# Performance work log

Hardware: AMD Instinct MI355X
Metric: run time of the kernel (lower is better)

## Reference

```python
import jax, jax.numpy as jnp
import numpy as np

B, N, D = 8, 4096, 3


def setup_inputs() -> dict:
    key = jax.random.key(0)
    k1, k2, k3 = jax.random.split(key, 3)
    pred1 = jax.random.normal(k1, (B, N, D), dtype=jnp.float32)
    pred2 = jax.random.normal(k2, (B, N, D), dtype=jnp.float32)
    # weighted adjacency in [0,1); column sums (degrees) strictly > 0
    A = jax.random.uniform(k3, (B, N, N), dtype=jnp.float32)
    return {"pred1": pred1, "pred2": pred2, "A": A}


def _centroid(x, A):
    # torch code computes neighbours[b,i,d] = sum_j A[b,i,j] * x[b,j,d]
    # and divides by num_neighbours[b,i] = sum over dim=1 of A (column sums).
    deg = jnp.sum(A, axis=1)                     # [B, N] column sums
    neigh = jnp.einsum('bij,bjd->bid', A, x)     # [B, N, D] row-aggregation
    return neigh / deg[..., None]


def reference(pred1, pred2, A):
    lap1 = pred1 - _centroid(pred1, A)
    lap2 = pred2 - _centroid(pred2, A)
    d = lap2 - lap1
    return jnp.sum(d * d)
```

## Files before the change

### kernel.cpp

```cpp
#include <hip/hip_runtime.h>

#define BB 8
#define NN 4096
#define TPB 256
#define NCB 32
#define SC 128
#define NRB 4
#define RR 1024
#define TSTEPS (RR / 16)
#define NDSLAB (NRB * 4)


__global__ __launch_bounds__(256) void k_init(const float* __restrict__ p1,
                                              const float* __restrict__ p2,
                                              float* __restrict__ q,
                                              float* __restrict__ neighp,
                                              float* __restrict__ degp,
                                              float* __restrict__ out,
                                              int atomic_mode) {
    int i = blockIdx.x * 256 + threadIdx.x;
    if (i < BB * NN * 3) q[i] = p2[i] - p1[i];
    if (atomic_mode) {
        if (i < BB * NN * 3) neighp[i] = 0.0f;
        if (i < BB * NN) degp[i] = 0.0f;
    }
    if (i == 0) out[0] = 0.0f;
}

__global__ __launch_bounds__(TPB, 4) void k_main(const float* __restrict__ A,
                                                 const float* __restrict__ q,
                                                 float* __restrict__ neighp,
                                                 float* __restrict__ degp,
                                                 int atomic_mode) {
    const int lane = threadIdx.x & 63;
    const int w    = threadIdx.x >> 6;
    const int rs   = lane >> 4;
    const int cq   = lane & 15;

    int bid = blockIdx.x;
    const int cb = bid & (NCB - 1); bid >>= 5;
    const int rb = bid & (NRB - 1); bid >>= 2;
    const int b  = bid;

    const int col  = cb * SC + cq * 8;
    const int row0 = rb * RR + w * 4 + rs;

    const float* qp = q + (size_t)b * NN * 3 + (size_t)col * 3;
    const float4 v0 = *(const float4*)(qp + 0);
    const float4 v1 = *(const float4*)(qp + 4);
    const float4 v2 = *(const float4*)(qp + 8);
    const float4 v3 = *(const float4*)(qp + 12);
    const float4 v4 = *(const float4*)(qp + 16);
    const float4 v5 = *(const float4*)(qp + 20);

    const float* Ap = A + (size_t)b * NN * NN + (size_t)row0 * NN + col;

    float4 dgA = make_float4(0.f, 0.f, 0.f, 0.f);
    float4 dgB = make_float4(0.f, 0.f, 0.f, 0.f);

    float* npbase = atomic_mode ? (neighp + (size_t)b * NN * 3)
                                : (neighp + (size_t)(cb * BB + b) * NN * 3);

#pragma unroll 2
    for (int t = 0; t < TSTEPS; ++t) {
        const float4 a1 = *(const float4*)(Ap);
        const float4 a2 = *(const float4*)(Ap + 4);
        Ap += (size_t)16 * NN;

        dgA.x += a1.x; dgA.y += a1.y; dgA.z += a1.z; dgA.w += a1.w;
        dgB.x += a2.x; dgB.y += a2.y; dgB.z += a2.z; dgB.w += a2.w;

        float n0 = a1.x * v0.x + a1.y * v0.w + a1.z * v1.z + a1.w * v2.y +
                   a2.x * v3.x + a2.y * v3.w + a2.z * v4.z + a2.w * v5.y;
        float n1 = a1.x * v0.y + a1.y * v1.x + a1.z * v1.w + a1.w * v2.z +
                   a2.x * v3.y + a2.y * v4.x + a2.z * v4.w + a2.w * v5.z;
        float n2 = a1.x * v0.z + a1.y * v1.y + a1.z * v2.x + a1.w * v2.w +
                   a2.x * v3.z + a2.y * v4.y + a2.z * v5.x + a2.w * v5.w;

#pragma unroll
        for (int s = 1; s < 16; s <<= 1) {
            n0 += __shfl_xor(n0, s, 64);
            n1 += __shfl_xor(n1, s, 64);
            n2 += __shfl_xor(n2, s, 64);
        }
        if (cq == 0) {
            const int row = row0 + t * 16;
            float* p = npbase + (size_t)row * 3;
            if (atomic_mode) {
                atomicAdd(&p[0], n0); atomicAdd(&p[1], n1); atomicAdd(&p[2], n2);
            } else {
                p[0] = n0; p[1] = n1; p[2] = n2;
            }
        }
    }

#pragma unroll
    for (int s = 16; s < 64; s <<= 1) {
        dgA.x += __shfl_xor(dgA.x, s, 64); dgA.y += __shfl_xor(dgA.y, s, 64);
        dgA.z += __shfl_xor(dgA.z, s, 64); dgA.w += __shfl_xor(dgA.w, s, 64);
        dgB.x += __shfl_xor(dgB.x, s, 64); dgB.y += __shfl_xor(dgB.y, s, 64);
        dgB.z += __shfl_xor(dgB.z, s, 64); dgB.w += __shfl_xor(dgB.w, s, 64);
    }
    if (rs == 0) {
        if (atomic_mode) {
            float* dp = degp + (size_t)b * NN + col;
            atomicAdd(&dp[0], dgA.x); atomicAdd(&dp[1], dgA.y);
            atomicAdd(&dp[2], dgA.z); atomicAdd(&dp[3], dgA.w);
            atomicAdd(&dp[4], dgB.x); atomicAdd(&dp[5], dgB.y);
            atomicAdd(&dp[6], dgB.z); atomicAdd(&dp[7], dgB.w);
        } else {
            float* dp = degp + ((size_t)(rb * 4 + w) * BB + b) * NN + col;
            *(float4*)(dp + 0) = dgA;
            *(float4*)(dp + 4) = dgB;
        }
    }
}

__global__ __launch_bounds__(256) void k_final(const float* __restrict__ q,
                                               const float* __restrict__ neighp,
                                               const float* __restrict__ degp,
                                               int nslab, int ncb,
                                               float* __restrict__ out) {
    __shared__ float dredN[4][64][3];
    __shared__ float dredD[4][64];
    const int lane = threadIdx.x & 63;
    const int qi   = threadIdx.x >> 6;
    const int R    = blockIdx.x * 64 + lane;
    const int b    = R / NN;
    const int i    = R - b * NN;

    float n0 = 0.f, n1 = 0.f, n2 = 0.f;
    for (int c = qi; c < ncb; c += 4) {
        const float* p = neighp + ((size_t)(c * BB + b) * NN + i) * 3;
        n0 += p[0]; n1 += p[1]; n2 += p[2];
    }
    dredN[qi][lane][0] = n0; dredN[qi][lane][1] = n1; dredN[qi][lane][2] = n2;

    float d0 = 0.f;
    for (int s = qi; s < nslab; s += 4)
        d0 += degp[((size_t)s * BB + b) * NN + i];
    dredD[qi][lane] = d0;
    __syncthreads();

    if (qi == 0) {
        const float deg = dredD[0][lane] + dredD[1][lane] + dredD[2][lane] + dredD[3][lane];
        const float inv = 1.0f / deg;
        const float nd0 = dredN[0][lane][0] + dredN[1][lane][0] + dredN[2][lane][0] + dredN[3][lane][0];
        const float nd1 = dredN[0][lane][1] + dredN[1][lane][1] + dredN[2][lane][1] + dredN[3][lane][1];
        const float nd2 = dredN[0][lane][2] + dredN[1][lane][2] + dredN[2][lane][2] + dredN[3][lane][2];

        const float c0 = q[(size_t)R * 3 + 0] - nd0 * inv;
        const float c1 = q[(size_t)R * 3 + 1] - nd1 * inv;
        const float c2 = q[(size_t)R * 3 + 2] - nd2 * inv;
        float acc = c0 * c0 + c1 * c1 + c2 * c2;
#pragma unroll
        for (int sft = 32; sft > 0; sft >>= 1) acc += __shfl_down(acc, sft, 64);
        if (lane == 0) atomicAdd(out, acc);
    }
}

extern "C" void kernel_launch(void* const* d_in, const int* in_sizes, int n_in,
                              void* d_out, int out_size, void* d_ws, size_t ws_size,
                              hipStream_t stream) {
    const float* pred1 = (const float*)d_in[0];
    const float* pred2 = (const float*)d_in[1];
    const float* A     = (const float*)d_in[2];
    float* out = (float*)d_out;

    float* q      = (float*)d_ws;
    float* neighp = q + (size_t)BB * NN * 3;
    float* degp   = neighp + (size_t)NCB * BB * NN * 3;

    const size_t need_partial =
        ((size_t)BB * NN * 3 + (size_t)NCB * BB * NN * 3 + (size_t)NDSLAB * BB * NN) *
        sizeof(float);
    const int atomic_mode = (ws_size < need_partial) ? 1 : 0;
    const int nslab = atomic_mode ? 1 : NDSLAB;
    const int ncb   = atomic_mode ? 1 : NCB;

    k_init<<<(BB * NN * 3 + 255) / 256, 256, 0, stream>>>(pred1, pred2, q, neighp,
                                                          degp, out, atomic_mode);
    k_main<<<BB * NRB * NCB, TPB, 0, stream>>>(A, q, neighp, degp, atomic_mode);
    k_final<<<(BB * NN) / 64, 256, 0, stream>>>(q, neighp, degp, nslab, ncb, out);
}
```

Before: 119.6 us.

## Widen column tiles, fuse q computation into main kernel, use nontemporal loads

Each thread now processes 16 columns instead of 8, with 16 column blocks and 8 row blocks, which halves the number of partial neighbour slabs written and read. The q = pred2 - pred1 difference is computed inline in k_main and k_final, so the q workspace buffer is removed and k_init shrinks to a single block in non-atomic mode. Loads of A use nontemporal hints to avoid polluting the cache on a single streaming pass. The cost is higher register use (48 q values and 16 degree accumulators), so the occupancy hint drops from 4 to 3 blocks.

```diff
diff --git a/kernel.cpp b/kernel.cpp
--- a/kernel.cpp
+++ b/kernel.cpp
@@ -3,23 +3,21 @@
 #define BB 8
 #define NN 4096
 #define TPB 256
-#define NCB 32
-#define SC 128
-#define NRB 4
-#define RR 1024
+#define NCB 16
+#define SC 256
+#define NRB 8
+#define RR 512
 #define TSTEPS (RR / 16)
 #define NDSLAB (NRB * 4)
 
+typedef float f32x4 __attribute__((ext_vector_type(4)));
 
-__global__ __launch_bounds__(256) void k_init(const float* __restrict__ p1,
-                                              const float* __restrict__ p2,
-                                              float* __restrict__ q,
-                                              float* __restrict__ neighp,
+
+__global__ __launch_bounds__(256) void k_init(float* __restrict__ neighp,
                                               float* __restrict__ degp,
                                               float* __restrict__ out,
                                               int atomic_mode) {
     int i = blockIdx.x * 256 + threadIdx.x;
-    if (i < BB * NN * 3) q[i] = p2[i] - p1[i];
     if (atomic_mode) {
         if (i < BB * NN * 3) neighp[i] = 0.0f;
         if (i < BB * NN) degp[i] = 0.0f;
@@ -27,8 +25,9 @@
     if (i == 0) out[0] = 0.0f;
 }
 
-__global__ __launch_bounds__(TPB, 4) void k_main(const float* __restrict__ A,
-                                                 const float* __restrict__ q,
+__global__ __launch_bounds__(TPB, 3) void k_main(const float* __restrict__ A,
+                                                 const float* __restrict__ p1,
+                                                 const float* __restrict__ p2,
                                                  float* __restrict__ neighp,
                                                  float* __restrict__ degp,
                                                  int atomic_mode) {
@@ -38,45 +37,56 @@
     const int cq   = lane & 15;
 
     int bid = blockIdx.x;
-    const int cb = bid & (NCB - 1); bid >>= 5;
-    const int rb = bid & (NRB - 1); bid >>= 2;
+    const int cb = bid & (NCB - 1); bid >>= 4;
+    const int rb = bid & (NRB - 1); bid >>= 3;
     const int b  = bid;
 
-    const int col  = cb * SC + cq * 8;
+    const int col  = cb * SC + cq * 16;
     const int row0 = rb * RR + w * 4 + rs;
 
-    const float* qp = q + (size_t)b * NN * 3 + (size_t)col * 3;
-    const float4 v0 = *(const float4*)(qp + 0);
-    const float4 v1 = *(const float4*)(qp + 4);
-    const float4 v2 = *(const float4*)(qp + 8);
-    const float4 v3 = *(const float4*)(qp + 12);
-    const float4 v4 = *(const float4*)(qp + 16);
-    const float4 v5 = *(const float4*)(qp + 20);
+    const size_t qbase = ((size_t)b * NN + col) * 3;
+    float qf[48];
+#pragma unroll
+    for (int k = 0; k < 12; ++k) {
+        const f32x4 t1 = *(const f32x4*)(p1 + qbase + 4 * k);
+        const f32x4 t2 = *(const f32x4*)(p2 + qbase + 4 * k);
+        qf[4 * k + 0] = t2[0] - t1[0];
+        qf[4 * k + 1] = t2[1] - t1[1];
+        qf[4 * k + 2] = t2[2] - t1[2];
+        qf[4 * k + 3] = t2[3] - t1[3];
+    }
 
     const float* Ap = A + (size_t)b * NN * NN + (size_t)row0 * NN + col;
 
-    float4 dgA = make_float4(0.f, 0.f, 0.f, 0.f);
-    float4 dgB = make_float4(0.f, 0.f, 0.f, 0.f);
+    float dg[16];
+#pragma unroll
+    for (int c = 0; c < 16; ++c) dg[c] = 0.0f;
 
     float* npbase = atomic_mode ? (neighp + (size_t)b * NN * 3)
                                 : (neighp + (size_t)(cb * BB + b) * NN * 3);
 
 #pragma unroll 2
     for (int t = 0; t < TSTEPS; ++t) {
-        const float4 a1 = *(const float4*)(Ap);
-        const float4 a2 = *(const float4*)(Ap + 4);
+        const f32x4 a0 = __builtin_nontemporal_load((const f32x4*)(Ap + 0));
+        const f32x4 a1 = __builtin_nontemporal_load((const f32x4*)(Ap + 4));
+        const f32x4 a2 = __builtin_nontemporal_load((const f32x4*)(Ap + 8));
+        const f32x4 a3 = __builtin_nontemporal_load((const f32x4*)(Ap + 12));
         Ap += (size_t)16 * NN;
 
-        dgA.x += a1.x; dgA.y += a1.y; dgA.z += a1.z; dgA.w += a1.w;
-        dgB.x += a2.x; dgB.y += a2.y; dgB.z += a2.z; dgB.w += a2.w;
+        float av[16];
+#pragma unroll
+        for (int j = 0; j < 4; ++j) {
+            av[j] = a0[j]; av[4 + j] = a1[j]; av[8 + j] = a2[j]; av[12 + j] = a3[j];
+        }
 
-        float n0 = a1.x * v0.x + a1.y * v0.w + a1.z * v1.z + a1.w * v2.y +
-                   a2.x * v3.x + a2.y * v3.w + a2.z * v4.z + a2.w * v5.y;
-        float n1 = a1.x * v0.y + a1.y * v1.x + a1.z * v1.w + a1.w * v2.z +
-                   a2.x * v3.y + a2.y * v4.x + a2.z * v4.w + a2.w * v5.z;
-        float n2 = a1.x * v0.z + a1.y * v1.y + a1.z * v2.x + a1.w * v2.w +
-                   a2.x * v3.z + a2.y * v4.y + a2.z * v5.x + a2.w * v5.w;
-
+        float n0 = 0.f, n1 = 0.f, n2 = 0.f;
+#pragma unroll
+        for (int c = 0; c < 16; ++c) {
+            dg[c] += av[c];
+            n0 += av[c] * qf[3 * c + 0];
+            n1 += av[c] * qf[3 * c + 1];
+            n2 += av[c] * qf[3 * c + 2];
+        }
 #pragma unroll
         for (int s = 1; s < 16; s <<= 1) {
             n0 += __shfl_xor(n0, s, 64);
@@ -96,27 +106,29 @@
 
 #pragma unroll
     for (int s = 16; s < 64; s <<= 1) {
-        dgA.x += __shfl_xor(dgA.x, s, 64); dgA.y += __shfl_xor(dgA.y, s, 64);
-        dgA.z += __shfl_xor(dgA.z, s, 64); dgA.w += __shfl_xor(dgA.w, s, 64);
-        dgB.x += __shfl_xor(dgB.x, s, 64); dgB.y += __shfl_xor(dgB.y, s, 64);
-        dgB.z += __shfl_xor(dgB.z, s, 64); dgB.w += __shfl_xor(dgB.w, s, 64);
+#pragma unroll
+        for (int c = 0; c < 16; ++c) dg[c] += __shfl_xor(dg[c], s, 64);
     }
     if (rs == 0) {
         if (atomic_mode) {
             float* dp = degp + (size_t)b * NN + col;
-            atomicAdd(&dp[0], dgA.x); atomicAdd(&dp[1], dgA.y);
-            atomicAdd(&dp[2], dgA.z); atomicAdd(&dp[3], dgA.w);
-            atomicAdd(&dp[4], dgB.x); atomicAdd(&dp[5], dgB.y);
-            atomicAdd(&dp[6], dgB.z); atomicAdd(&dp[7], dgB.w);
+#pragma unroll
+            for (int c = 0; c < 16; ++c) atomicAdd(&dp[c], dg[c]);
         } else {
             float* dp = degp + ((size_t)(rb * 4 + w) * BB + b) * NN + col;
-            *(float4*)(dp + 0) = dgA;
-            *(float4*)(dp + 4) = dgB;
+#pragma unroll
+            for (int k = 0; k < 4; ++k) {
+                f32x4 v;
+                v[0] = dg[4 * k + 0]; v[1] = dg[4 * k + 1];
+                v[2] = dg[4 * k + 2]; v[3] = dg[4 * k + 3];
+                *(f32x4*)(dp + 4 * k) = v;
+            }
         }
     }
 }
 
-__global__ __launch_bounds__(256) void k_final(const float* __restrict__ q,
+__global__ __launch_bounds__(256) void k_final(const float* __restrict__ p1,
+                                               const float* __restrict__ p2,
                                                const float* __restrict__ neighp,
                                                const float* __restrict__ degp,
                                                int nslab, int ncb,
@@ -149,9 +161,9 @@
         const float nd1 = dredN[0][lane][1] + dredN[1][lane][1] + dredN[2][lane][1] + dredN[3][lane][1];
         const float nd2 = dredN[0][lane][2] + dredN[1][lane][2] + dredN[2][lane][2] + dredN[3][lane][2];
 
-        const float c0 = q[(size_t)R * 3 + 0] - nd0 * inv;
-        const float c1 = q[(size_t)R * 3 + 1] - nd1 * inv;
-        const float c2 = q[(size_t)R * 3 + 2] - nd2 * inv;
+        const float c0 = (p2[(size_t)R * 3 + 0] - p1[(size_t)R * 3 + 0]) - nd0 * inv;
+        const float c1 = (p2[(size_t)R * 3 + 1] - p1[(size_t)R * 3 + 1]) - nd1 * inv;
+        const float c2 = (p2[(size_t)R * 3 + 2] - p1[(size_t)R * 3 + 2]) - nd2 * inv;
         float acc = c0 * c0 + c1 * c1 + c2 * c2;
 #pragma unroll
         for (int sft = 32; sft > 0; sft >>= 1) acc += __shfl_down(acc, sft, 64);
@@ -167,19 +179,19 @@
     const float* A     = (const float*)d_in[2];
     float* out = (float*)d_out;
 
-    float* q      = (float*)d_ws;
-    float* neighp = q + (size_t)BB * NN * 3;
+    float* neighp = (float*)d_ws;
     float* degp   = neighp + (size_t)NCB * BB * NN * 3;
 
     const size_t need_partial =
-        ((size_t)BB * NN * 3 + (size_t)NCB * BB * NN * 3 + (size_t)NDSLAB * BB * NN) *
-        sizeof(float);
+        ((size_t)NCB * BB * NN * 3 + (size_t)NDSLAB * BB * NN) * sizeof(float);
     const int atomic_mode = (ws_size < need_partial) ? 1 : 0;
     const int nslab = atomic_mode ? 1 : NDSLAB;
     const int ncb   = atomic_mode ? 1 : NCB;
 
-    k_init<<<(BB * NN * 3 + 255) / 256, 256, 0, stream>>>(pred1, pred2, q, neighp,
-                                                          degp, out, atomic_mode);
-    k_main<<<BB * NRB * NCB, TPB, 0, stream>>>(A, q, neighp, degp, atomic_mode);
-    k_final<<<(BB * NN) / 64, 256, 0, stream>>>(q, neighp, degp, nslab, ncb, out);
+    const int init_grid = atomic_mode ? (BB * NN * 3 + 255) / 256 : 1;
+    k_init<<<init_grid, 256, 0, stream>>>(neighp, degp, out, atomic_mode);
+    k_main<<<BB * NRB * NCB, TPB, 0, stream>>>(A, pred1, pred2, neighp, degp,
+                                               atomic_mode);
+    k_final<<<(BB * NN) / 64, 256, 0, stream>>>(pred1, pred2, neighp, degp,
+                                                nslab, ncb, out);
 }
```

Measured after the change: 165.4 us. 1.38x slower.
